# Optimization experiments

Hardware: AMD Instinct MI355X
Metric: run time of the kernel (lower is better)

The kernel has to match this reference:

```python
import jax, jax.numpy as jnp
import numpy as np

B, L, NT = 4, 512, 20
H, DK, DM = 6, 10, 60  # heads, d_k, d_model (=embedding_dim+1)
ED = 59


def setup_inputs() -> dict:
    key = jax.random.key(0)
    ks = jax.random.split(key, 12)
    # event_seqs[..., 0] = event times (increasing), event_seqs[..., 1] = event type id stored as float
    times = jnp.cumsum(jax.random.uniform(ks[0], (B, L + 1)), axis=1)
    types = jax.random.randint(ks[1], (B, L + 1), 0, NT).astype(jnp.float32)
    event_seqs = jnp.stack([times, types], axis=-1)  # [B, L+1, 2]
    # causal (subsequent) mask, no padding -> lower-triangular [B, L, L]
    src_mask = jnp.broadcast_to(jnp.tril(jnp.ones((L, L), dtype=bool)), (B, L, L))
    w = lambda k, s: jax.random.normal(k, s, dtype=jnp.float32) * 0.1
    return dict(
        event_seqs=event_seqs, src_mask=src_mask,
        embed_w=w(ks[2], (ED, NT)),
        q_w=w(ks[3], (DM, DM)), q_b=jnp.zeros((DM,), jnp.float32),
        k_w=w(ks[4], (DM, DM)), k_b=jnp.zeros((DM,), jnp.float32),
        v_w=w(ks[5], (DM, DM)), v_b=jnp.zeros((DM,), jnp.float32),
        alpha_w=w(ks[6], (DK, DK * H // 2)), alpha_b=jnp.zeros((DK,), jnp.float32),
        gamma_w=w(ks[7], (DK, DK * H // 2)), gamma_b=jnp.zeros((DK,), jnp.float32),
        mu_w=w(ks[8], (DK, DM)), mu_b=jnp.zeros((DK,), jnp.float32),
    )


def reference(event_seqs, src_mask, embed_w, q_w, q_b, k_w, k_b, v_w, v_b,
              alpha_w, alpha_b, gamma_w, gamma_b, mu_w, mu_b):
    b = event_seqs.shape[0]
    # temporal feature: dt between consecutive events (ts padded with leading 0)
    ts = jnp.pad(event_seqs[:, :, 0], ((0, 0), (1, 0)))  # [B, T+1]
    dt = ts[:, 1:] - ts[:, :-1]                           # [B, T]
    temp_feat = dt[:, :-1, None]                          # [B, L, 1]
    types = event_seqs[:, :-1, 1].astype(jnp.int32)       # [B, L]
    type_feat = jax.nn.one_hot(types, NT, dtype=jnp.float32) @ embed_w.T  # [B, L, ED]
    feat = jnp.concatenate([temp_feat, type_feat], axis=-1)  # [B, L, DM]

    def heads(x, w, bias):
        return (x @ w.T + bias).reshape(b, L, H, DK).transpose(0, 2, 1, 3)  # [B,H,L,DK]

    q = heads(feat, q_w, q_b)
    k = heads(feat, k_w, k_b)
    v = heads(feat, v_w, v_b)

    mask4 = src_mask[:, None, :, :]  # [B,1,L,L]
    scores = jnp.einsum('bhid,bhjd->bhij', q, k) / np.sqrt(DK).astype(np.float32)
    scores = jnp.where(mask4, scores, -1e9)
    p_attn = jax.nn.softmax(scores, axis=-1)
    p_attn = jnp.where(mask4, p_attn, 0.0)               # [B,H,L,L]
    v_mu_pre = jnp.einsum('bhij,bhjd->bhid', p_attn, v)  # [B,H,L,DK]

    # per-pair attn * value, split heads in half (faithful to torch view semantics)
    prod = p_attn[..., None] * v[:, :, None, :, :]       # [B,H,L,L,DK]
    hh = H // 2
    x_alpha = prod[:, :hh].reshape(b, L, L, hh * DK)     # raw C-order reshape == torch .view
    x_gamma = prod[:, hh:].reshape(b, L, L, hh * DK)

    v_alpha = jax.nn.softplus(x_alpha @ alpha_w.T + alpha_b)          # Softplus(beta=1)
    v_gamma = jax.nn.softplus(10.0 * (x_gamma @ gamma_w.T + gamma_b)) / 10.0  # Softplus(beta=10)
    pair_mask = src_mask[..., None]                      # [B,L,L,1]
    v_alpha = jnp.where(pair_mask, v_alpha, 0.0)
    v_gamma = jnp.where(pair_mask, v_gamma, 0.0)

    v_mu = jax.nn.sigmoid(v_mu_pre.transpose(0, 2, 1, 3).reshape(b, L, DM) @ mu_w.T + mu_b)  # [B,L,DK]
    return (v_mu, v_alpha, v_gamma)
```

## Files before the change

kernel.cpp:

```cpp
#include <hip/hip_runtime.h>
#include <hip/hip_bf16.h>

#define BB 4
#define LL 512
#define NTYPES 20
#define HH 6
#define DKK 10
#define DMM 60
#define PROW 516
#define NWROW 516

__device__ __forceinline__ float softplus_fast(float x) {
    return fmaxf(x, 0.0f) + __logf(1.0f + __expf(-fabsf(x)));
}

__global__ __launch_bounds__(256) void ishp_qkv(
        const float* __restrict__ ev, const float* __restrict__ embed_w,
        const float* __restrict__ qw, const float* __restrict__ qb,
        const float* __restrict__ kw, const float* __restrict__ kb,
        const float* __restrict__ vw, const float* __restrict__ vb,
        const float* __restrict__ aw, const float* __restrict__ gw,
        float* __restrict__ q, float* __restrict__ kR, float* __restrict__ vR,
        float* __restrict__ Wbuf)
{
    int blk = blockIdx.x;
    int b = blk >> 6;
    int l0 = (blk & 63) * 8;
    __shared__ float sFeat[8][61];
    __shared__ float sv8[8][DMM];
    __shared__ int   sTyp[8];
    int t = threadIdx.x;

    if (t < 8) {
        int l = l0 + t;
        float t1 = ev[(b * (LL + 1) + l) * 2 + 0];
        float t0 = (l > 0) ? ev[(b * (LL + 1) + l - 1) * 2 + 0] : 0.0f;
        sFeat[t][0] = t1 - t0;
        sTyp[t] = (int)ev[(b * (LL + 1) + l) * 2 + 1];
    }
    __syncthreads();
    #pragma unroll
    for (int u = 0; u < 2; ++u) {
        int idx = u * 256 + t;
        if (idx < 472) {
            int l = idx / 59, c = idx - (idx / 59) * 59;
            sFeat[l][1 + c] = embed_w[c * NTYPES + sTyp[l]];
        }
    }
    __syncthreads();

    if (t < 180) {
        int which = t / DMM;
        int m = t - which * DMM;
        const float* w  = which == 0 ? qw : which == 1 ? kw : vw;
        const float* bs = which == 0 ? qb : which == 1 ? kb : vb;
        float bias = bs[m];
        float wr[DMM];
        #pragma unroll
        for (int c = 0; c < DMM; ++c) wr[c] = w[m * DMM + c];
        int h = m / DKK, d = m - h * DKK;
        #pragma unroll
        for (int s = 0; s < 8; ++s) {
            float acc = bias;
            #pragma unroll
            for (int c = 0; c < DMM; ++c) acc += sFeat[s][c] * wr[c];
            int l = l0 + s;
            size_t off = ((size_t)(b * HH + h) * LL + l) * DKK + d;
            if (which == 0)      q [off] = acc;
            else if (which == 1) kR[off] = acc;
            else { vR[off] = acc; sv8[s][m] = acc; }
        }
    }
    __syncthreads();

    if (t < 180) {
        int kk = t % 10;
        int u = t / 10;
        int h  = u % 3;
        int cc = (u / 3) % 3;
        int mat = u / 9;
        const float* w = mat ? gw : aw;
        float wr[DKK];
        #pragma unroll
        for (int d = 0; d < DKK; ++d) wr[d] = w[kk * 30 + cc * 10 + d];
        size_t rowbase = ((size_t)((((mat * 3 + cc) * 4 + b) * 3 + h) * 10 + kk)) * NWROW;
        #pragma unroll
        for (int s = 0; s < 8; ++s) {
            float acc = 0.0f;
            #pragma unroll
            for (int d = 0; d < DKK; ++d) acc += wr[d] * sv8[s][(h + 3 * mat) * DKK + d];
            int l = l0 + s;
            int slot = (l % 3) * 172 + l / 3;
            Wbuf[rowbase + slot] = acc;
        }
    }
}

__global__ __launch_bounds__(256) void ishp_attn(const float* __restrict__ q,
                                                 const float* __restrict__ kR,
                                                 const float* __restrict__ vR,
                                                 __hip_bfloat16* __restrict__ pbuf,
                                                 float* __restrict__ vmupre)
{
    __shared__ float sK[DKK * LL];
    __shared__ float sV[DKK * LL];
    int bh = blockIdx.x >> 5;
    int rg = blockIdx.x & 31;
    int tid = threadIdx.x;
    int lane = tid & 63;
    int wv = tid >> 6;

    const float2* k2 = reinterpret_cast<const float2*>(kR + (size_t)bh * DKK * LL);
    const float2* v2 = reinterpret_cast<const float2*>(vR + (size_t)bh * DKK * LL);
    #pragma unroll
    for (int u = 0; u < 10; ++u) {
        int idx = u * 256 + tid;
        int l = idx / 5, dp = idx % 5;
        float2 kv = k2[idx];
        sK[(2 * dp) * LL + l] = kv.x;
        sK[(2 * dp + 1) * LL + l] = kv.y;
        float2 vv = v2[idx];
        sV[(2 * dp) * LL + l] = vv.x;
        sV[(2 * dp + 1) * LL + l] = vv.y;
    }
    __syncthreads();

    const float scale = 0.31622776601683794f;

    #pragma unroll
    for (int sidx = 0; sidx < 2; ++sidx) {
        int P = rg * 8 + wv + 4 * sidx;
        #pragma unroll
        for (int half = 0; half < 2; ++half) {
            int i = half == 0 ? (511 - P) : P;
            float qr[DKK];
            #pragma unroll
            for (int d = 0; d < DKK; ++d) qr[d] = q[((size_t)bh * LL + i) * DKK + d];
            int nchunk = (i >> 6) + 1;

            float e[8];
            float S = 0.0f;
            #pragma unroll
            for (int c = 0; c < 8; ++c) {
                e[c] = 0.0f;
                if (c < nchunk) {
                    int j = c * 64 + lane;
                    float dot = 0.0f;
                    #pragma unroll
                    for (int d = 0; d < DKK; ++d) dot += qr[d] * sK[d * LL + j];
                    if (j <= i) e[c] = __expf(dot * scale);
                    S += e[c];
                }
            }
            #pragma unroll
            for (int off = 32; off >= 1; off >>= 1) S += __shfl_xor(S, off, 64);
            float inv = 1.0f / S;

            __hip_bfloat16* prow = pbuf + (size_t)(bh * LL + i) * PROW;
            #pragma unroll
            for (int c = 0; c < 8; ++c) {
                if (c < nchunk) {
                    int j = c * 64 + lane;
                    int slot = (j % 3) * 172 + j / 3;
                    if (j <= i) prow[slot] = __float2bfloat16(e[c] * inv);
                }
            }

            float acc[DKK];
            #pragma unroll
            for (int d = 0; d < DKK; ++d) acc[d] = 0.0f;
            #pragma unroll
            for (int c = 0; c < 8; ++c) {
                if (c < nchunk) {
                    int j = c * 64 + lane;
                    #pragma unroll
                    for (int d = 0; d < DKK; ++d) acc[d] += e[c] * sV[d * LL + j];
                }
            }
            #pragma unroll
            for (int d = 0; d < DKK; ++d) {
                float a = acc[d];
                #pragma unroll
                for (int off = 32; off >= 1; off >>= 1) a += __shfl_xor(a, off, 64);
                acc[d] = a;
            }
            if (lane == 0) {
                #pragma unroll
                for (int d = 0; d < DKK; ++d)
                    vmupre[((size_t)bh * LL + i) * DKK + d] = acc[d] * inv;
            }
        }
    }
}

__global__ __launch_bounds__(256) void ishp_ag(const __hip_bfloat16* __restrict__ pbuf,
                                               const float* __restrict__ Wbuf,
                                               const float* __restrict__ ab,
                                               const float* __restrict__ gb,
                                               const float* __restrict__ vmupre,
                                               const float* __restrict__ muw,
                                               const float* __restrict__ mub,
                                               float* __restrict__ out_mu,
                                               float* __restrict__ outA,
                                               float* __restrict__ outG)
{
    __shared__ float sA[2560];
    __shared__ float sG[2560];
    int tid = threadIdx.x;
    int pos = blockIdx.x * 256 + tid;
    int b  = pos >> 18;
    int i2 = (pos >> 9) & 511;
    int j2 = pos & 511;

    float ra[DKK], rg[DKK];
    if (j2 > i2) {
        #pragma unroll
        for (int kk = 0; kk < DKK; ++kk) { ra[kk] = 0.0f; rg[kk] = 0.0f; }
    } else {
        #pragma unroll
        for (int kk = 0; kk < DKK; ++kk) { ra[kk] = ab[kk]; rg[kk] = gb[kk]; }
        #pragma unroll
        for (int cc = 0; cc < 3; ++cc) {
            int u = 3 * j2 + cc;
            int sel = u >> 9;
            int j = u & 511;
            int hi = 3 * i2 + sel;
            int h = hi >> 9;
            int i = hi & 511;
            int jq = j / 3;
            int r = j - 3 * jq;
            int slot = r * 172 + jq;
            float pa = 0.0f, pg = 0.0f;
            if (j <= i) {
                pa = __bfloat162float(pbuf[(size_t)((b * HH + h) * LL + i) * PROW + slot]);
                pg = __bfloat162float(pbuf[(size_t)((b * HH + h + 3) * LL + i) * PROW + slot]);
            }
            const float* Wa = Wbuf + ((size_t)(((0 + cc) * 4 + b) * 3 + h) * 10) * NWROW + slot;
            const float* Wg = Wbuf + ((size_t)(((3 + cc) * 4 + b) * 3 + h) * 10) * NWROW + slot;
            #pragma unroll
            for (int kk = 0; kk < DKK; ++kk) {
                ra[kk] += pa * Wa[kk * NWROW];
                rg[kk] += pg * Wg[kk * NWROW];
            }
        }
        #pragma unroll
        for (int kk = 0; kk < DKK; ++kk) {
            ra[kk] = softplus_fast(ra[kk]);
            rg[kk] = softplus_fast(10.0f * rg[kk]) * 0.1f;
        }
    }
    #pragma unroll
    for (int kk = 0; kk < DKK; ++kk) { sA[tid * 10 + kk] = ra[kk]; sG[tid * 10 + kk] = rg[kk]; }
    __syncthreads();

    size_t base = (size_t)blockIdx.x * 2560;
    #pragma unroll
    for (int it = 0; it < 3; ++it) {
        int idx = it * 1024 + tid * 4;
        if (idx < 2560) {
            *reinterpret_cast<float4*>(outA + base + idx) = *reinterpret_cast<const float4*>(&sA[idx]);
            *reinterpret_cast<float4*>(outG + base + idx) = *reinterpret_cast<const float4*>(&sG[idx]);
        }
    }

    if (blockIdx.x < 8) {
        int mpos = blockIdx.x * 256 + tid;
        int mb = mpos >> 9, ml = mpos & 511;
        float y[DKK];
        #pragma unroll
        for (int kk = 0; kk < DKK; ++kk) y[kk] = mub[kk];
        for (int c = 0; c < DMM; ++c) {
            int h = c / DKK, d = c - h * DKK;
            float xc = vmupre[((mb * HH + h) * LL + ml) * DKK + d];
            #pragma unroll
            for (int kk = 0; kk < DKK; ++kk) y[kk] += xc * muw[kk * DMM + c];
        }
        #pragma unroll
        for (int kk = 0; kk < DKK; ++kk)
            out_mu[(size_t)mpos * DKK + kk] = 1.0f / (1.0f + __expf(-y[kk]));
    }
}

extern "C" void kernel_launch(void* const* d_in, const int* in_sizes, int n_in,
                              void* d_out, int out_size, void* d_ws, size_t ws_size,
                              hipStream_t stream) {
    const void *ev = 0, *emb = 0, *muw = 0;
    const void *w3[3] = {0, 0, 0}, *b3[3] = {0, 0, 0};
    const void *w300[2] = {0, 0};
    const void *b10[3] = {0, 0, 0};
    int n3 = 0, nb3 = 0, n300 = 0, n10 = 0;
    for (int i = 0; i < n_in; ++i) {
        int s = in_sizes[i];
        if      (s == 4104) ev  = d_in[i];
        else if (s == 1180) emb = d_in[i];
        else if (s == 600)  muw = d_in[i];
        else if (s == 3600) { if (n3  < 3) w3[n3++]   = d_in[i]; }
        else if (s == 60)   { if (nb3 < 3) b3[nb3++]  = d_in[i]; }
        else if (s == 300)  { if (n300< 2) w300[n300++]=d_in[i]; }
        else if (s == 10)   { if (n10 < 3) b10[n10++] = d_in[i]; }
    }

    float* ws = (float*)d_ws;
    float* q = ws;
    float* kR = q + 122880;
    float* vR = kR + 122880;
    float* vmupre = vR + 122880;
    float* Wbuf = vmupre + 122880;
    __hip_bfloat16* pbuf = (__hip_bfloat16*)(Wbuf + 371520);

    float* out = (float*)d_out;
    float* out_mu = out;
    float* out_a  = out + 20480;
    float* out_g  = out + 20480 + 10485760;

    ishp_qkv<<<(BB * LL) / 8, 256, 0, stream>>>((const float*)ev, (const float*)emb,
        (const float*)w3[0], (const float*)b3[0],
        (const float*)w3[1], (const float*)b3[1],
        (const float*)w3[2], (const float*)b3[2],
        (const float*)w300[0], (const float*)w300[1],
        q, kR, vR, Wbuf);
    ishp_attn<<<BB * HH * 32, 256, 0, stream>>>(q, kR, vR, pbuf, vmupre);
    ishp_ag<<<(BB * LL * LL) / 256, 256, 0, stream>>>(pbuf, Wbuf,
        (const float*)b10[0], (const float*)b10[1], vmupre,
        (const float*)muw, (const float*)b10[2], out_mu, out_a, out_g);
}
```

Baseline: 56.08 us.

## Fuse paired causal rows in attention and store K/V row-major for vector LDS loads

The attention kernel now processes the high and low query rows of each balanced pair together. Each K and V shared-memory row is loaded once and used for both dot products and both accumulations. The shared layout changes from d-major to row-major with a 12-float stride, so each lane reads its key or value with float4/float2 loads instead of ten scalar loads. This cuts LDS traffic and instruction count, in exchange for higher register pressure from two sets of q, e and accumulator arrays, plus possible LDS bank conflicts from the strided layout.

```diff
diff --git a/kernel.cpp b/kernel.cpp
--- a/kernel.cpp
+++ b/kernel.cpp
@@ -9,6 +9,7 @@
 #define DMM 60
 #define PROW 516
 #define NWROW 516
+#define KROW 12
 
 __device__ __forceinline__ float softplus_fast(float x) {
     return fmaxf(x, 0.0f) + __logf(1.0f + __expf(-fabsf(x)));
@@ -102,8 +103,8 @@
                                                  __hip_bfloat16* __restrict__ pbuf,
                                                  float* __restrict__ vmupre)
 {
-    __shared__ float sK[DKK * LL];
-    __shared__ float sV[DKK * LL];
+    __shared__ float sK[LL * KROW];
+    __shared__ float sV[LL * KROW];
     int bh = blockIdx.x >> 5;
     int rg = blockIdx.x & 31;
     int tid = threadIdx.x;
@@ -115,13 +116,13 @@
     #pragma unroll
     for (int u = 0; u < 10; ++u) {
         int idx = u * 256 + tid;
-        int l = idx / 5, dp = idx % 5;
+        int l = idx / 5, dp = idx - (idx / 5) * 5;
         float2 kv = k2[idx];
-        sK[(2 * dp) * LL + l] = kv.x;
-        sK[(2 * dp + 1) * LL + l] = kv.y;
+        sK[l * KROW + 2 * dp]     = kv.x;
+        sK[l * KROW + 2 * dp + 1] = kv.y;
         float2 vv = v2[idx];
-        sV[(2 * dp) * LL + l] = vv.x;
-        sV[(2 * dp + 1) * LL + l] = vv.y;
+        sV[l * KROW + 2 * dp]     = vv.x;
+        sV[l * KROW + 2 * dp + 1] = vv.y;
     }
     __syncthreads();
 
@@ -130,64 +131,96 @@
     #pragma unroll
     for (int sidx = 0; sidx < 2; ++sidx) {
         int P = rg * 8 + wv + 4 * sidx;
-        #pragma unroll
-        for (int half = 0; half < 2; ++half) {
-            int i = half == 0 ? (511 - P) : P;
-            float qr[DKK];
-            #pragma unroll
-            for (int d = 0; d < DKK; ++d) qr[d] = q[((size_t)bh * LL + i) * DKK + d];
-            int nchunk = (i >> 6) + 1;
-
-            float e[8];
-            float S = 0.0f;
-            #pragma unroll
-            for (int c = 0; c < 8; ++c) {
-                e[c] = 0.0f;
-                if (c < nchunk) {
-                    int j = c * 64 + lane;
-                    float dot = 0.0f;
-                    #pragma unroll
-                    for (int d = 0; d < DKK; ++d) dot += qr[d] * sK[d * LL + j];
-                    if (j <= i) e[c] = __expf(dot * scale);
-                    S += e[c];
+        int i_hi = 511 - P, i_lo = P;
+        float qh[DKK], ql[DKK];
+        #pragma unroll
+        for (int d = 0; d < DKK; ++d) {
+            qh[d] = q[((size_t)bh * LL + i_hi) * DKK + d];
+            ql[d] = q[((size_t)bh * LL + i_lo) * DKK + d];
+        }
+        int nch_h = (i_hi >> 6) + 1;
+        int nch_l = (i_lo >> 6) + 1;
+
+        float eh[8], el[8];
+        float Sh = 0.0f, Sl = 0.0f;
+        #pragma unroll
+        for (int c = 0; c < 8; ++c) {
+            eh[c] = 0.0f; el[c] = 0.0f;
+            if (c < nch_h) {
+                int j = c * 64 + lane;
+                const float* kr = &sK[j * KROW];
+                float4 k0 = *reinterpret_cast<const float4*>(kr);
+                float4 k1 = *reinterpret_cast<const float4*>(kr + 4);
+                float2 kv2 = *reinterpret_cast<const float2*>(kr + 8);
+                float dh = qh[0] * k0.x; dh += qh[1] * k0.y; dh += qh[2] * k0.z; dh += qh[3] * k0.w;
+                dh += qh[4] * k1.x; dh += qh[5] * k1.y; dh += qh[6] * k1.z; dh += qh[7] * k1.w;
+                dh += qh[8] * kv2.x; dh += qh[9] * kv2.y;
+                if (j <= i_hi) eh[c] = __expf(dh * scale);
+                Sh += eh[c];
+                if (c < nch_l) {
+                    float dl = ql[0] * k0.x; dl += ql[1] * k0.y; dl += ql[2] * k0.z; dl += ql[3] * k0.w;
+                    dl += ql[4] * k1.x; dl += ql[5] * k1.y; dl += ql[6] * k1.z; dl += ql[7] * k1.w;
+                    dl += ql[8] * kv2.x; dl += ql[9] * kv2.y;
+                    if (j <= i_lo) el[c] = __expf(dl * scale);
+                    Sl += el[c];
                 }
             }
-            #pragma unroll
-            for (int off = 32; off >= 1; off >>= 1) S += __shfl_xor(S, off, 64);
-            float inv = 1.0f / S;
-
-            __hip_bfloat16* prow = pbuf + (size_t)(bh * LL + i) * PROW;
-            #pragma unroll
-            for (int c = 0; c < 8; ++c) {
-                if (c < nchunk) {
-                    int j = c * 64 + lane;
-                    int slot = (j % 3) * 172 + j / 3;
-                    if (j <= i) prow[slot] = __float2bfloat16(e[c] * inv);
+        }
+        #pragma unroll
+        for (int off = 32; off >= 1; off >>= 1) {
+            Sh += __shfl_xor(Sh, off, 64);
+            Sl += __shfl_xor(Sl, off, 64);
+        }
+        float inv_h = 1.0f / Sh, inv_l = 1.0f / Sl;
+
+        __hip_bfloat16* prow_h = pbuf + (size_t)(bh * LL + i_hi) * PROW;
+        __hip_bfloat16* prow_l = pbuf + (size_t)(bh * LL + i_lo) * PROW;
+        #pragma unroll
+        for (int c = 0; c < 8; ++c) {
+            if (c < nch_h) {
+                int j = c * 64 + lane;
+                int slot = (j % 3) * 172 + j / 3;
+                if (j <= i_hi) prow_h[slot] = __float2bfloat16(eh[c] * inv_h);
+                if (c < nch_l && j <= i_lo) prow_l[slot] = __float2bfloat16(el[c] * inv_l);
+            }
+        }
+
+        float ah[DKK], al[DKK];
+        #pragma unroll
+        for (int d = 0; d < DKK; ++d) { ah[d] = 0.0f; al[d] = 0.0f; }
+        #pragma unroll
+        for (int c = 0; c < 8; ++c) {
+            if (c < nch_h) {
+                int j = c * 64 + lane;
+                const float* vr = &sV[j * KROW];
+                float4 v0 = *reinterpret_cast<const float4*>(vr);
+                float4 v1 = *reinterpret_cast<const float4*>(vr + 4);
+                float2 vv2 = *reinterpret_cast<const float2*>(vr + 8);
+                ah[0] += eh[c] * v0.x; ah[1] += eh[c] * v0.y; ah[2] += eh[c] * v0.z; ah[3] += eh[c] * v0.w;
+                ah[4] += eh[c] * v1.x; ah[5] += eh[c] * v1.y; ah[6] += eh[c] * v1.z; ah[7] += eh[c] * v1.w;
+                ah[8] += eh[c] * vv2.x; ah[9] += eh[c] * vv2.y;
+                if (c < nch_l) {
+                    al[0] += el[c] * v0.x; al[1] += el[c] * v0.y; al[2] += el[c] * v0.z; al[3] += el[c] * v0.w;
+                    al[4] += el[c] * v1.x; al[5] += el[c] * v1.y; al[6] += el[c] * v1.z; al[7] += el[c] * v1.w;
+                    al[8] += el[c] * vv2.x; al[9] += el[c] * vv2.y;
                 }
             }
-
-            float acc[DKK];
-            #pragma unroll
-            for (int d = 0; d < DKK; ++d) acc[d] = 0.0f;
-            #pragma unroll
-            for (int c = 0; c < 8; ++c) {
-                if (c < nchunk) {
-                    int j = c * 64 + lane;
-                    #pragma unroll
-                    for (int d = 0; d < DKK; ++d) acc[d] += e[c] * sV[d * LL + j];
-                }
-            }
+        }
+        #pragma unroll
+        for (int d = 0; d < DKK; ++d) {
+            float a0 = ah[d], a1 = al[d];
+            #pragma unroll
+            for (int off = 32; off >= 1; off >>= 1) {
+                a0 += __shfl_xor(a0, off, 64);
+                a1 += __shfl_xor(a1, off, 64);
+            }
+            ah[d] = a0; al[d] = a1;
+        }
+        if (lane == 0) {
             #pragma unroll
             for (int d = 0; d < DKK; ++d) {
-                float a = acc[d];
-                #pragma unroll
-                for (int off = 32; off >= 1; off >>= 1) a += __shfl_xor(a, off, 64);
-                acc[d] = a;
-            }
-            if (lane == 0) {
-                #pragma unroll
-                for (int d = 0; d < DKK; ++d)
-                    vmupre[((size_t)bh * LL + i) * DKK + d] = acc[d] * inv;
+                vmupre[((size_t)bh * LL + i_hi) * DKK + d] = ah[d] * inv_h;
+                vmupre[((size_t)bh * LL + i_lo) * DKK + d] = al[d] * inv_l;
             }
         }
     }
```

After: 53.20 us. 1.05x faster.

## Single-pass attention storing unnormalized probs with per-row inverse sums deferred

Applied to the files above, without the earlier changes.

The attention kernel now handles four query rows per wave in one pass over key chunks, using row-major K/V in shared memory read as vector loads. It writes unnormalized exp values to the probability buffer and stores each row's 1/sum in a new buffer. The downstream kernel applies that normalization when it reads the values. This removes the second pass and the re-read of K/V per row, but it adds an extra global load per pair in the large alpha/gamma kernel and uses more registers. Storing unnormalized exps in bf16 could also change rounding.

```diff
diff --git a/kernel.cpp b/kernel.cpp
--- a/kernel.cpp
+++ b/kernel.cpp
@@ -9,6 +9,7 @@
 #define DMM 60
 #define PROW 516
 #define NWROW 516
+#define KROW 12
 
 __device__ __forceinline__ float softplus_fast(float x) {
     return fmaxf(x, 0.0f) + __logf(1.0f + __expf(-fabsf(x)));
@@ -100,10 +101,11 @@
                                                  const float* __restrict__ kR,
                                                  const float* __restrict__ vR,
                                                  __hip_bfloat16* __restrict__ pbuf,
+                                                 float* __restrict__ invSbuf,
                                                  float* __restrict__ vmupre)
 {
-    __shared__ float sK[DKK * LL];
-    __shared__ float sV[DKK * LL];
+    __shared__ float sK[LL * KROW];
+    __shared__ float sV[LL * KROW];
     int bh = blockIdx.x >> 5;
     int rg = blockIdx.x & 31;
     int tid = threadIdx.x;
@@ -115,85 +117,97 @@
     #pragma unroll
     for (int u = 0; u < 10; ++u) {
         int idx = u * 256 + tid;
-        int l = idx / 5, dp = idx % 5;
+        int l = idx / 5, dp = idx - (idx / 5) * 5;
         float2 kv = k2[idx];
-        sK[(2 * dp) * LL + l] = kv.x;
-        sK[(2 * dp + 1) * LL + l] = kv.y;
+        sK[l * KROW + 2 * dp]     = kv.x;
+        sK[l * KROW + 2 * dp + 1] = kv.y;
         float2 vv = v2[idx];
-        sV[(2 * dp) * LL + l] = vv.x;
-        sV[(2 * dp + 1) * LL + l] = vv.y;
+        sV[l * KROW + 2 * dp]     = vv.x;
+        sV[l * KROW + 2 * dp + 1] = vv.y;
     }
     __syncthreads();
 
     const float scale = 0.31622776601683794f;
 
-    #pragma unroll
-    for (int sidx = 0; sidx < 2; ++sidx) {
-        int P = rg * 8 + wv + 4 * sidx;
-        #pragma unroll
-        for (int half = 0; half < 2; ++half) {
-            int i = half == 0 ? (511 - P) : P;
-            float qr[DKK];
-            #pragma unroll
-            for (int d = 0; d < DKK; ++d) qr[d] = q[((size_t)bh * LL + i) * DKK + d];
-            int nchunk = (i >> 6) + 1;
-
-            float e[8];
-            float S = 0.0f;
-            #pragma unroll
-            for (int c = 0; c < 8; ++c) {
-                e[c] = 0.0f;
-                if (c < nchunk) {
-                    int j = c * 64 + lane;
-                    float dot = 0.0f;
-                    #pragma unroll
-                    for (int d = 0; d < DKK; ++d) dot += qr[d] * sK[d * LL + j];
-                    if (j <= i) e[c] = __expf(dot * scale);
-                    S += e[c];
+    int P0 = rg * 8 + wv;
+    int rows[4];
+    rows[0] = 511 - P0; rows[1] = P0; rows[2] = 507 - P0; rows[3] = P0 + 4;
+
+    float qr[4][DKK];
+    int nch[4];
+    #pragma unroll
+    for (int r = 0; r < 4; ++r) {
+        #pragma unroll
+        for (int d = 0; d < DKK; ++d) qr[r][d] = q[((size_t)bh * LL + rows[r]) * DKK + d];
+        nch[r] = (rows[r] >> 6) + 1;
+    }
+    float S[4] = {0.f, 0.f, 0.f, 0.f};
+    float acc[4][DKK];
+    #pragma unroll
+    for (int r = 0; r < 4; ++r)
+        #pragma unroll
+        for (int d = 0; d < DKK; ++d) acc[r][d] = 0.0f;
+
+    int nmax = nch[0];
+    for (int c = 0; c < nmax; ++c) {
+        int j = c * 64 + lane;
+        int slot = (j % 3) * 172 + j / 3;
+        const float* kr = &sK[j * KROW];
+        float4 k0 = *reinterpret_cast<const float4*>(kr);
+        float4 k1 = *reinterpret_cast<const float4*>(kr + 4);
+        float2 kv2 = *reinterpret_cast<const float2*>(kr + 8);
+        const float* vr = &sV[j * KROW];
+        float4 v0 = *reinterpret_cast<const float4*>(vr);
+        float4 v1 = *reinterpret_cast<const float4*>(vr + 4);
+        float2 vv2 = *reinterpret_cast<const float2*>(vr + 8);
+        #pragma unroll
+        for (int r = 0; r < 4; ++r) {
+            if (c < nch[r]) {
+                float dt = qr[r][0] * k0.x; dt += qr[r][1] * k0.y; dt += qr[r][2] * k0.z; dt += qr[r][3] * k0.w;
+                dt += qr[r][4] * k1.x; dt += qr[r][5] * k1.y; dt += qr[r][6] * k1.z; dt += qr[r][7] * k1.w;
+                dt += qr[r][8] * kv2.x; dt += qr[r][9] * kv2.y;
+                float e = 0.0f;
+                if (j <= rows[r]) {
+                    e = __expf(dt * scale);
+                    pbuf[(size_t)(bh * LL + rows[r]) * PROW + slot] = __float2bfloat16(e);
                 }
+                S[r] += e;
+                acc[r][0] += e * v0.x; acc[r][1] += e * v0.y; acc[r][2] += e * v0.z; acc[r][3] += e * v0.w;
+                acc[r][4] += e * v1.x; acc[r][5] += e * v1.y; acc[r][6] += e * v1.z; acc[r][7] += e * v1.w;
+                acc[r][8] += e * vv2.x; acc[r][9] += e * vv2.y;
             }
-            #pragma unroll
-            for (int off = 32; off >= 1; off >>= 1) S += __shfl_xor(S, off, 64);
-            float inv = 1.0f / S;
-
-            __hip_bfloat16* prow = pbuf + (size_t)(bh * LL + i) * PROW;
-            #pragma unroll
-            for (int c = 0; c < 8; ++c) {
-                if (c < nchunk) {
-                    int j = c * 64 + lane;
-                    int slot = (j % 3) * 172 + j / 3;
-                    if (j <= i) prow[slot] = __float2bfloat16(e[c] * inv);
-                }
-            }
-
-            float acc[DKK];
-            #pragma unroll
-            for (int d = 0; d < DKK; ++d) acc[d] = 0.0f;
-            #pragma unroll
-            for (int c = 0; c < 8; ++c) {
-                if (c < nchunk) {
-                    int j = c * 64 + lane;
-                    #pragma unroll
-                    for (int d = 0; d < DKK; ++d) acc[d] += e[c] * sV[d * LL + j];
-                }
-            }
-            #pragma unroll
-            for (int d = 0; d < DKK; ++d) {
-                float a = acc[d];
-                #pragma unroll
-                for (int off = 32; off >= 1; off >>= 1) a += __shfl_xor(a, off, 64);
-                acc[d] = a;
-            }
-            if (lane == 0) {
-                #pragma unroll
-                for (int d = 0; d < DKK; ++d)
-                    vmupre[((size_t)bh * LL + i) * DKK + d] = acc[d] * inv;
-            }
+        }
+    }
+    #pragma unroll
+    for (int r = 0; r < 4; ++r)
+        #pragma unroll
+        for (int off = 32; off >= 1; off >>= 1) S[r] += __shfl_xor(S[r], off, 64);
+    float inv[4];
+    #pragma unroll
+    for (int r = 0; r < 4; ++r) inv[r] = 1.0f / S[r];
+
+    #pragma unroll
+    for (int r = 0; r < 4; ++r)
+        #pragma unroll
+        for (int d = 0; d < DKK; ++d) {
+            float a = acc[r][d];
+            #pragma unroll
+            for (int off = 32; off >= 1; off >>= 1) a += __shfl_xor(a, off, 64);
+            acc[r][d] = a;
+        }
+    if (lane == 0) {
+        #pragma unroll
+        for (int r = 0; r < 4; ++r) {
+            invSbuf[(size_t)bh * LL + rows[r]] = inv[r];
+            #pragma unroll
+            for (int d = 0; d < DKK; ++d)
+                vmupre[((size_t)bh * LL + rows[r]) * DKK + d] = acc[r][d] * inv[r];
         }
     }
 }
 
 __global__ __launch_bounds__(256) void ishp_ag(const __hip_bfloat16* __restrict__ pbuf,
+                                               const float* __restrict__ invSbuf,
                                                const float* __restrict__ Wbuf,
                                                const float* __restrict__ ab,
                                                const float* __restrict__ gb,
@@ -232,8 +246,10 @@
             int slot = r * 172 + jq;
             float pa = 0.0f, pg = 0.0f;
             if (j <= i) {
-                pa = __bfloat162float(pbuf[(size_t)((b * HH + h) * LL + i) * PROW + slot]);
-                pg = __bfloat162float(pbuf[(size_t)((b * HH + h + 3) * LL + i) * PROW + slot]);
+                float ea = __bfloat162float(pbuf[(size_t)((b * HH + h) * LL + i) * PROW + slot]);
+                float eg = __bfloat162float(pbuf[(size_t)((b * HH + h + 3) * LL + i) * PROW + slot]);
+                pa = ea * invSbuf[(size_t)(b * HH + h) * LL + i];
+                pg = eg * invSbuf[(size_t)(b * HH + h + 3) * LL + i];
             }
             const float* Wa = Wbuf + ((size_t)(((0 + cc) * 4 + b) * 3 + h) * 10) * NWROW + slot;
             const float* Wg = Wbuf + ((size_t)(((3 + cc) * 4 + b) * 3 + h) * 10) * NWROW + slot;
@@ -306,7 +322,8 @@
     float* vR = kR + 122880;
     float* vmupre = vR + 122880;
     float* Wbuf = vmupre + 122880;
-    __hip_bfloat16* pbuf = (__hip_bfloat16*)(Wbuf + 371520);
+    float* invSbuf = Wbuf + 371520;
+    __hip_bfloat16* pbuf = (__hip_bfloat16*)(invSbuf + 12288);
 
     float* out = (float*)d_out;
     float* out_mu = out;
@@ -319,8 +336,8 @@
         (const float*)w3[2], (const float*)b3[2],
         (const float*)w300[0], (const float*)w300[1],
         q, kR, vR, Wbuf);
-    ishp_attn<<<BB * HH * 32, 256, 0, stream>>>(q, kR, vR, pbuf, vmupre);
-    ishp_ag<<<(BB * LL * LL) / 256, 256, 0, stream>>>(pbuf, Wbuf,
+    ishp_attn<<<BB * HH * 32, 256, 0, stream>>>(q, kR, vR, pbuf, invSbuf, vmupre);
+    ishp_ag<<<(BB * LL * LL) / 256, 256, 0, stream>>>(pbuf, invSbuf, Wbuf,
         (const float*)b10[0], (const float*)b10[1], vmupre,
         (const float*)muw, (const float*)b10[2], out_mu, out_a, out_g);
 }
```

Measured after the change: 53.81 us. 4.1% less time.
